# Optimization experiments

Hardware: AMD Instinct MI355X
Metric: run time of the kernel (lower is better)

## Reference

```python
import jax, jax.numpy as jnp
import numpy as np

B, L, S, H = 2, 256, 384, 768
Tc, Dc = 16, 50
WV, WD = 20000, 100
CV = 128
NEG = -1e30


def _lstm_scan(x, Wih, Whh, bih, bhh):
    # x: [N, T, D] -> hs: [N, T, Hc]; torch LSTM gate order i,f,g,o
    N = x.shape[0]
    Hc = Whh.shape[1]
    h0 = jnp.zeros((N, Hc), x.dtype)

    def step(carry, xt):
        h, c = carry
        g = xt @ Wih.T + h @ Whh.T + bih + bhh  # [N, 4Hc]
        i, f, gg, o = jnp.split(g, 4, axis=-1)
        i = jax.nn.sigmoid(i)
        f = jax.nn.sigmoid(f)
        gg = jnp.tanh(gg)
        o = jax.nn.sigmoid(o)
        c = f * c + i * gg
        h = o * jnp.tanh(c)
        return (h, c), h

    _, hs = jax.lax.scan(step, (h0, h0), jnp.swapaxes(x, 0, 1))
    return jnp.swapaxes(hs, 0, 1)


def setup_inputs() -> dict:
    key = jax.random.key(0)
    ks = jax.random.split(key, 10)
    bert_emb = jax.random.normal(ks[0], (B, S, H), jnp.float32)
    pieces2word = jax.random.randint(ks[1], (B, L, S), 0, 2, jnp.int32)
    word_ids = jax.random.randint(ks[2], (B, L), 0, WV, jnp.int32)
    char_count = jax.random.randint(ks[3], (B, L), 1, Tc + 1, jnp.int32)
    char_ids = jax.random.randint(ks[4], (B, L, Tc), 0, CV, jnp.int32)
    # mask consistent with ragged char lengths (first char_count positions valid)
    token_masks_char = (jnp.arange(Tc)[None, None, :] < char_count[..., None]).astype(jnp.int32)
    word_table = jax.random.normal(ks[5], (WV, WD), jnp.float32) * 0.02
    char_table = jax.random.normal(ks[6], (CV, Dc), jnp.float32) * 0.02
    sc = 1.0 / np.sqrt(Dc)

    def lstm_w(k):
        a, b, c, d = jax.random.split(k, 4)
        return (jax.random.uniform(a, (4 * Dc, Dc), jnp.float32, -sc, sc),
                jax.random.uniform(b, (4 * Dc, Dc), jnp.float32, -sc, sc),
                jax.random.uniform(c, (4 * Dc,), jnp.float32, -sc, sc),
                jax.random.uniform(d, (4 * Dc,), jnp.float32, -sc, sc))

    Wih_f, Whh_f, bih_f, bhh_f = lstm_w(ks[7])
    Wih_b, Whh_b, bih_b, bhh_b = lstm_w(ks[8])
    return dict(bert_emb=bert_emb, pieces2word=pieces2word, word_ids=word_ids,
                char_count=char_count, char_ids=char_ids, token_masks_char=token_masks_char,
                word_table=word_table, char_table=char_table,
                Wih_f=Wih_f, Whh_f=Whh_f, bih_f=bih_f, bhh_f=bhh_f,
                Wih_b=Wih_b, Whh_b=Whh_b, bih_b=bih_b, bhh_b=bhh_b)


def reference(bert_emb, pieces2word, word_ids, char_count, char_ids, token_masks_char,
              word_table, char_table, Wih_f, Whh_f, bih_f, bhh_f, Wih_b, Whh_b, bih_b, bhh_b):
    # --- piece2word max pool (expand + masked_fill(min) + max over pieces) ---
    minv = jnp.min(bert_emb)
    # [B, L, S, H] intermediate, as in the original expand
    masked = jnp.where(pieces2word[..., None] != 0, bert_emb[:, None, :, :], minv)
    word_reps = jnp.max(masked, axis=2)  # [B, L, H]
    # dropouts are identity in eval mode

    # --- word embedding lookup ---
    word_embed = word_table[word_ids]  # [B, L, WD]

    # --- char bi-LSTM with packed-sequence semantics ---
    lens = jnp.maximum(char_count.reshape(-1), 1)  # char_count[char_count==0]=1
    x = char_table[char_ids.reshape(B * L, Tc)]  # [N, Tc, Dc]
    h_fwd = _lstm_scan(x, Wih_f, Whh_f, bih_f, bhh_f)
    # reverse each sequence within its valid length for the backward direction
    t = jnp.arange(Tc)[None, :]
    idx = jnp.where(t < lens[:, None], lens[:, None] - 1 - t, t)  # [N, Tc]
    x_rev = jnp.take_along_axis(x, idx[..., None], axis=1)
    h_bwd = _lstm_scan(x_rev, Wih_b, Whh_b, bih_b, bhh_b)
    h_bwd = jnp.take_along_axis(h_bwd, idx[..., None], axis=1)  # back to original order
    h = jnp.concatenate([h_fwd, h_bwd], axis=-1)  # [N, Tc, 2*Dc]
    valid = (t < lens[:, None])[..., None]
    h = jnp.where(valid, h, 0.0)  # pad_packed_sequence zero-pads beyond length
    h = h.reshape(B, L, Tc, 2 * Dc)

    # --- combine(..., 'max'): masked max over ragged char groups ---
    m = jnp.where(token_masks_char[..., None] == 0, NEG, 0.0)
    sup = jnp.max(m + h, axis=2)  # [B, L, 2*Dc]
    sup = jnp.where(sup == NEG, 0.0, sup)

    return jnp.concatenate([word_reps, word_embed, sup], axis=-1)  # [B, L, H+WD+2*Dc]
```

## Files before the change

### kernel.cpp

```cpp
#include <hip/hip_runtime.h>
#include <float.h>

#define Bb 2
#define Ll 256
#define Ss 384
#define Hh 768
#define Tc 16
#define Dc 50
#define WD 100
#define CV 128
#define NG 200
#define OUTC 968


__device__ inline float tanh_fast(float x) {
    float e = __expf(2.f * x);
    return 1.f - 2.f / (e + 1.f);
}
__device__ inline float sigmoid_fast(float x) {
    return 1.f / (1.f + __expf(-x));
}


__global__ __launch_bounds__(256) void kernel1(
        const float* __restrict__ bert, const float* __restrict__ char_table,
        const float* __restrict__ Wih_f, const float* __restrict__ bih_f, const float* __restrict__ bhh_f,
        const float* __restrict__ Wih_b, const float* __restrict__ bih_b, const float* __restrict__ bhh_b,
        float* __restrict__ minp, float* __restrict__ xpt) {
    int blk = blockIdx.x, tid = threadIdx.x;
    if (blk < 128) {
        const int n4 = (Bb * Ss * Hh) / 4;
        const float4* b4 = (const float4*)bert;
        float m = FLT_MAX;
        for (int i = blk * 256 + tid; i < n4; i += 128 * 256) {
            float4 v = b4[i];
            m = fminf(m, fminf(fminf(v.x, v.y), fminf(v.z, v.w)));
        }
        #pragma unroll
        for (int off = 32; off; off >>= 1) m = fminf(m, __shfl_down(m, off, 64));
        __shared__ float red[4];
        if ((tid & 63) == 0) red[tid >> 6] = m;
        __syncthreads();
        if (tid == 0) minp[blk] = fminf(fminf(red[0], red[1]), fminf(red[2], red[3]));
    } else {
        int idx = blk - 128;
        int dir = idx >> 3, c0 = (idx & 7) * 16;
        const float* Wih = dir ? Wih_b : Wih_f;
        const float* bih = dir ? bih_b : bih_f;
        const float* bhh = dir ? bhh_b : bhh_f;
        __shared__ float ct[16][Dc];
        for (int e = tid; e < 16 * Dc; e += 256)
            ((float*)ct)[e] = char_table[c0 * Dc + e];
        __syncthreads();
        if (tid < NG) {
            float w[Dc];
            #pragma unroll
            for (int j = 0; j < Dc; j++) w[j] = Wih[tid * Dc + j];
            float bias = bih[tid] + bhh[tid];
            for (int cid = 0; cid < 16; cid++) {
                float a = bias;
                #pragma unroll
                for (int j = 0; j < Dc; j++) a += w[j] * ct[cid][j];
                xpt[(dir * CV + c0 + cid) * NG + tid] = a;
            }
        }
    }
}


__global__ __launch_bounds__(256, 4) void kernel_lstm(
        const int* __restrict__ char_ids, const int* __restrict__ char_count,
        const float* __restrict__ Whh_f, const float* __restrict__ Whh_b,
        const float* __restrict__ xpt, float* __restrict__ out) {
    __shared__ __align__(16) char smem[13888];
    int blk = blockIdx.x, tid = threadIdx.x;

    float (*xg)[NG] = (float (*)[NG])smem;
    float* gs  = (float*)(smem + 12800);
    float* hs  = (float*)(smem + 13600);
    int*   scid = (int*)(smem + 13808);

    int n = blk >> 1, dir = blk & 1;
    const float* Whh = dir ? Whh_b : Whh_f;

    int len = char_count[n];
    if (len < 1) len = 1;
    if (tid < Tc) {
        int t = tid;
        int st = dir ? (t < len ? len - 1 - t : t) : t;
        scid[t] = char_ids[n * Tc + st];
    }
    if (tid < 52) hs[tid] = 0.f;
    __syncthreads();

    for (int e = tid; e < Tc * (NG / 4); e += 256) {
        int t = e / 50, q = e - t * 50;
        ((float4*)xg[t])[q] = ((const float4*)&xpt[(dir * CV + scid[t]) * NG])[q];
    }
    int wrow = tid < NG ? tid : NG - 1;
    bool istanh = (tid >= 100 && tid < 150);
    float w[52];
    #pragma unroll
    for (int j = 0; j < Dc; j++) w[j] = Whh[wrow * Dc + j];
    w[50] = 0.f; w[51] = 0.f;
    __syncthreads();

    float c = 0.f, maxv = -FLT_MAX;
    for (int t = 0; t < Tc; t++) {
        #pragma unroll
        for (int j = 0; j < 52; j++) asm volatile("" : "+v"(w[j]));
        if (tid < NG) {
            float g = xg[t][tid];
            #pragma unroll
            for (int j = 0; j < 52; j += 4) {
                float4 hv = *(const float4*)&hs[j];
                g += hv.x * w[j] + hv.y * w[j+1] + hv.z * w[j+2] + hv.w * w[j+3];
            }
            gs[tid] = istanh ? tanh_fast(g) : sigmoid_fast(g);
        }
        __syncthreads();
        if (tid < Dc) {
            float si = gs[tid];
            float sf = gs[tid + 50];
            float tg = gs[tid + 100];
            float so = gs[tid + 150];
            c = sf * c + si * tg;
            float h = so * tanh_fast(c);
            hs[tid] = h;
            if (t < len) maxv = fmaxf(maxv, h);
        }
        __syncthreads();
    }
    if (tid < Dc)
        out[(size_t)n * OUTC + (Hh + WD) + dir * Dc + tid] = maxv;
}


__global__ __launch_bounds__(256, 2) void kernel_word(
        const float* __restrict__ bert, const int* __restrict__ p2w,
        const float* __restrict__ minp,
        const int* __restrict__ word_ids, const float* __restrict__ word_table,
        float* __restrict__ out) {
    __shared__ __align__(16) float sm[Ss][8];
    __shared__ __align__(16) float sacc[4][8][128];
    __shared__ float sminv;
    int blk = blockIdx.x, tid = threadIdx.x;

    if (blk < 384) {
        int idx = blk;
        int hc  = idx % 6;
        int lt  = (idx / 6) & 31;
        int b   = idx / 192;
        int l0  = lt * 8;

        const int* pm = p2w + ((size_t)(b * Ll + l0)) * Ss;
        for (int e = tid; e < 8 * Ss; e += 256) {
            int r = e & 7, s = e >> 3;
            sm[s][r] = pm[r * Ss + s] ? 0.f : -FLT_MAX;
        }
        if (tid < 64) {
            float m = fminf(minp[tid], minp[tid + 64]);
            #pragma unroll
            for (int off = 32; off; off >>= 1) m = fminf(m, __shfl_down(m, off, 64));
            if (tid == 0) sminv = m;
        }
        __syncthreads();

        int w    = tid >> 6;
        int lane = tid & 63;
        int s0 = w * 96;

        const float2* bb2 = (const float2*)(bert + (size_t)b * Ss * Hh) + hc * 64 + lane;
        float2 acc[8];
        #pragma unroll
        for (int r = 0; r < 8; r++) { acc[r].x = -FLT_MAX; acc[r].y = -FLT_MAX; }

        for (int jo = 0; jo < 96; jo += 8) {
            float2 v[8];
            #pragma unroll
            for (int k = 0; k < 8; k++) v[k] = bb2[(size_t)(s0 + jo + k) * 384];
            #pragma unroll
            for (int k = 0; k < 8; k++) {
                int j = s0 + jo + k;
                float4 q0 = *(const float4*)&sm[j][0];
                float4 q1 = *(const float4*)&sm[j][4];
                acc[0].x = fmaxf(acc[0].x, v[k].x + q0.x);
                acc[0].y = fmaxf(acc[0].y, v[k].y + q0.x);
                acc[1].x = fmaxf(acc[1].x, v[k].x + q0.y);
                acc[1].y = fmaxf(acc[1].y, v[k].y + q0.y);
                acc[2].x = fmaxf(acc[2].x, v[k].x + q0.z);
                acc[2].y = fmaxf(acc[2].y, v[k].y + q0.z);
                acc[3].x = fmaxf(acc[3].x, v[k].x + q0.w);
                acc[3].y = fmaxf(acc[3].y, v[k].y + q0.w);
                acc[4].x = fmaxf(acc[4].x, v[k].x + q1.x);
                acc[4].y = fmaxf(acc[4].y, v[k].y + q1.x);
                acc[5].x = fmaxf(acc[5].x, v[k].x + q1.y);
                acc[5].y = fmaxf(acc[5].y, v[k].y + q1.y);
                acc[6].x = fmaxf(acc[6].x, v[k].x + q1.z);
                acc[6].y = fmaxf(acc[6].y, v[k].y + q1.z);
                acc[7].x = fmaxf(acc[7].x, v[k].x + q1.w);
                acc[7].y = fmaxf(acc[7].y, v[k].y + q1.w);
            }
        }
        #pragma unroll
        for (int r = 0; r < 8; r++)
            *(float2*)&sacc[w][r][lane * 2] = acc[r];
        __syncthreads();

        float mv = sminv;
        for (int e = tid; e < 8 * 128; e += 256) {
            int r = e >> 7, cx = e & 127;
            float m = fmaxf(fmaxf(sacc[0][r][cx], sacc[1][r][cx]),
                            fmaxf(sacc[2][r][cx], sacc[3][r][cx]));
            if (m == -FLT_MAX) m = mv;
            out[((size_t)(b * Ll + l0 + r)) * OUTC + hc * 128 + cx] = m;
        }
    } else {
        for (int i = (blk - 384) * 256 + tid; i < Bb * Ll * WD; i += 64 * 256) {
            int bl = i / WD, d = i - bl * WD;
            out[(size_t)bl * OUTC + Hh + d] = word_table[(size_t)word_ids[bl] * WD + d];
        }
    }
}

extern "C" void kernel_launch(void* const* d_in, const int* in_sizes, int n_in,
                              void* d_out, int out_size, void* d_ws, size_t ws_size,
                              hipStream_t stream) {
    const float* bert       = (const float*)d_in[0];
    const int*   p2w        = (const int*)d_in[1];
    const int*   word_ids   = (const int*)d_in[2];
    const int*   char_count = (const int*)d_in[3];
    const int*   char_ids   = (const int*)d_in[4];
    const float* word_table = (const float*)d_in[6];
    const float* char_table = (const float*)d_in[7];
    const float* Wih_f = (const float*)d_in[8];
    const float* Whh_f = (const float*)d_in[9];
    const float* bih_f = (const float*)d_in[10];
    const float* bhh_f = (const float*)d_in[11];
    const float* Wih_b = (const float*)d_in[12];
    const float* Whh_b = (const float*)d_in[13];
    const float* bih_b = (const float*)d_in[14];
    const float* bhh_b = (const float*)d_in[15];
    float* out = (float*)d_out;

    float* minp = (float*)d_ws;
    float* xpt  = minp + 128;

    kernel1<<<144, 256, 0, stream>>>(
        bert, char_table, Wih_f, bih_f, bhh_f, Wih_b, bih_b, bhh_b,
        minp, xpt);
    kernel_lstm<<<1024, 256, 0, stream>>>(
        char_ids, char_count, Whh_f, Whh_b, xpt, out);
    kernel_word<<<448, 256, 0, stream>>>(
        bert, p2w, minp, word_ids, word_table, out);
}
```

Measured before the change: 128.7 us.

## Broadcast LSTM hidden state via readlane and halve word-tile rows

Every wavefront in the LSTM recurrence now computes the cell and hidden state redundantly for lanes 0-49. Each thread gets the hidden vector through readlane broadcasts instead of from a shared-memory buffer, which removes one block barrier per time step. The gate buffer is double-buffered so a single barrier per step is enough. The dot product is split across four accumulators. The word max-pool kernel processes 4 words per block instead of 8, doubling the block count for more parallelism, at the cost of reloading bert columns more times.

```diff
diff --git a/kernel.cpp b/kernel.cpp
--- a/kernel.cpp
+++ b/kernel.cpp
@@ -72,25 +72,21 @@
         const int* __restrict__ char_ids, const int* __restrict__ char_count,
         const float* __restrict__ Whh_f, const float* __restrict__ Whh_b,
         const float* __restrict__ xpt, float* __restrict__ out) {
-    __shared__ __align__(16) char smem[13888];
+    __shared__ __align__(16) float xg[Tc][NG];
+    __shared__ __align__(16) float gsb[2][NG];
+    __shared__ int scid[Tc];
+
     int blk = blockIdx.x, tid = threadIdx.x;
-
-    float (*xg)[NG] = (float (*)[NG])smem;
-    float* gs  = (float*)(smem + 12800);
-    float* hs  = (float*)(smem + 13600);
-    int*   scid = (int*)(smem + 13808);
-
     int n = blk >> 1, dir = blk & 1;
     const float* Whh = dir ? Whh_b : Whh_f;
+    int lane = tid & 63;
 
     int len = char_count[n];
     if (len < 1) len = 1;
     if (tid < Tc) {
-        int t = tid;
-        int st = dir ? (t < len ? len - 1 - t : t) : t;
-        scid[t] = char_ids[n * Tc + st];
-    }
-    if (tid < 52) hs[tid] = 0.f;
+        int st = dir ? (tid < len ? len - 1 - tid : tid) : tid;
+        scid[tid] = char_ids[n * Tc + st];
+    }
     __syncthreads();
 
     for (int e = tid; e < Tc * (NG / 4); e += 256) {
@@ -99,63 +95,61 @@
     }
     int wrow = tid < NG ? tid : NG - 1;
     bool istanh = (tid >= 100 && tid < 150);
-    float w[52];
+    float w[50];
     #pragma unroll
-    for (int j = 0; j < Dc; j++) w[j] = Whh[wrow * Dc + j];
-    w[50] = 0.f; w[51] = 0.f;
+    for (int j = 0; j < 50; j++) w[j] = Whh[wrow * 50 + j];
     __syncthreads();
 
-    float c = 0.f, maxv = -FLT_MAX;
+    int ch = lane < 50 ? lane : 49;
+    float c = 0.f, h = 0.f, maxv = -FLT_MAX;
     for (int t = 0; t < Tc; t++) {
-        #pragma unroll
-        for (int j = 0; j < 52; j++) asm volatile("" : "+v"(w[j]));
-        if (tid < NG) {
-            float g = xg[t][tid];
-            #pragma unroll
-            for (int j = 0; j < 52; j += 4) {
-                float4 hv = *(const float4*)&hs[j];
-                g += hv.x * w[j] + hv.y * w[j+1] + hv.z * w[j+2] + hv.w * w[j+3];
-            }
-            gs[tid] = istanh ? tanh_fast(g) : sigmoid_fast(g);
-        }
-        __syncthreads();
-        if (tid < Dc) {
-            float si = gs[tid];
-            float sf = gs[tid + 50];
-            float tg = gs[tid + 100];
-            float so = gs[tid + 150];
-            c = sf * c + si * tg;
-            float h = so * tanh_fast(c);
-            hs[tid] = h;
-            if (t < len) maxv = fmaxf(maxv, h);
-        }
-        __syncthreads();
-    }
-    if (tid < Dc)
+        int hb = __float_as_int(h);
+        float g0 = xg[t][wrow], g1 = 0.f, g2 = 0.f, g3 = 0.f;
+        #pragma unroll
+        for (int j = 0; j < 48; j += 4) {
+            g0 = fmaf(__int_as_float(__builtin_amdgcn_readlane(hb, j)),     w[j],     g0);
+            g1 = fmaf(__int_as_float(__builtin_amdgcn_readlane(hb, j + 1)), w[j + 1], g1);
+            g2 = fmaf(__int_as_float(__builtin_amdgcn_readlane(hb, j + 2)), w[j + 2], g2);
+            g3 = fmaf(__int_as_float(__builtin_amdgcn_readlane(hb, j + 3)), w[j + 3], g3);
+        }
+        g0 = fmaf(__int_as_float(__builtin_amdgcn_readlane(hb, 48)), w[48], g0);
+        g1 = fmaf(__int_as_float(__builtin_amdgcn_readlane(hb, 49)), w[49], g1);
+        float g = (g0 + g1) + (g2 + g3);
+        if (tid < NG)
+            gsb[t & 1][tid] = istanh ? tanh_fast(g) : sigmoid_fast(g);
+        __syncthreads();
+        float si = gsb[t & 1][ch];
+        float sf = gsb[t & 1][ch + 50];
+        float tg = gsb[t & 1][ch + 100];
+        float so = gsb[t & 1][ch + 150];
+        c = sf * c + si * tg;
+        h = so * tanh_fast(c);
+        if (t < len) maxv = fmaxf(maxv, h);
+    }
+    if (tid < 50)
         out[(size_t)n * OUTC + (Hh + WD) + dir * Dc + tid] = maxv;
 }
 
 
-__global__ __launch_bounds__(256, 2) void kernel_word(
+__global__ __launch_bounds__(256) void kernel_word(
         const float* __restrict__ bert, const int* __restrict__ p2w,
         const float* __restrict__ minp,
         const int* __restrict__ word_ids, const float* __restrict__ word_table,
         float* __restrict__ out) {
-    __shared__ __align__(16) float sm[Ss][8];
-    __shared__ __align__(16) float sacc[4][8][128];
+    __shared__ __align__(16) float sm[Ss][4];
+    __shared__ __align__(16) float sacc[4][4][128];
     __shared__ float sminv;
     int blk = blockIdx.x, tid = threadIdx.x;
 
-    if (blk < 384) {
-        int idx = blk;
-        int hc  = idx % 6;
-        int lt  = (idx / 6) & 31;
-        int b   = idx / 192;
-        int l0  = lt * 8;
+    if (blk < 768) {
+        int hc  = blk % 6;
+        int lt  = (blk / 6) & 63;
+        int b   = blk / 384;
+        int l0  = lt * 4;
 
         const int* pm = p2w + ((size_t)(b * Ll + l0)) * Ss;
-        for (int e = tid; e < 8 * Ss; e += 256) {
-            int r = e & 7, s = e >> 3;
+        for (int e = tid; e < 4 * Ss; e += 256) {
+            int r = e / Ss, s = e - r * Ss;
             sm[s][r] = pm[r * Ss + s] ? 0.f : -FLT_MAX;
         }
         if (tid < 64) {
@@ -171,9 +165,9 @@
         int s0 = w * 96;
 
         const float2* bb2 = (const float2*)(bert + (size_t)b * Ss * Hh) + hc * 64 + lane;
-        float2 acc[8];
-        #pragma unroll
-        for (int r = 0; r < 8; r++) { acc[r].x = -FLT_MAX; acc[r].y = -FLT_MAX; }
+        float2 acc[4];
+        #pragma unroll
+        for (int r = 0; r < 4; r++) { acc[r].x = -FLT_MAX; acc[r].y = -FLT_MAX; }
 
         for (int jo = 0; jo < 96; jo += 8) {
             float2 v[8];
@@ -182,33 +176,24 @@
             #pragma unroll
             for (int k = 0; k < 8; k++) {
                 int j = s0 + jo + k;
-                float4 q0 = *(const float4*)&sm[j][0];
-                float4 q1 = *(const float4*)&sm[j][4];
-                acc[0].x = fmaxf(acc[0].x, v[k].x + q0.x);
-                acc[0].y = fmaxf(acc[0].y, v[k].y + q0.x);
-                acc[1].x = fmaxf(acc[1].x, v[k].x + q0.y);
-                acc[1].y = fmaxf(acc[1].y, v[k].y + q0.y);
-                acc[2].x = fmaxf(acc[2].x, v[k].x + q0.z);
-                acc[2].y = fmaxf(acc[2].y, v[k].y + q0.z);
-                acc[3].x = fmaxf(acc[3].x, v[k].x + q0.w);
-                acc[3].y = fmaxf(acc[3].y, v[k].y + q0.w);
-                acc[4].x = fmaxf(acc[4].x, v[k].x + q1.x);
-                acc[4].y = fmaxf(acc[4].y, v[k].y + q1.x);
-                acc[5].x = fmaxf(acc[5].x, v[k].x + q1.y);
-                acc[5].y = fmaxf(acc[5].y, v[k].y + q1.y);
-                acc[6].x = fmaxf(acc[6].x, v[k].x + q1.z);
-                acc[6].y = fmaxf(acc[6].y, v[k].y + q1.z);
-                acc[7].x = fmaxf(acc[7].x, v[k].x + q1.w);
-                acc[7].y = fmaxf(acc[7].y, v[k].y + q1.w);
+                float4 q = *(const float4*)&sm[j][0];
+                acc[0].x = fmaxf(acc[0].x, v[k].x + q.x);
+                acc[0].y = fmaxf(acc[0].y, v[k].y + q.x);
+                acc[1].x = fmaxf(acc[1].x, v[k].x + q.y);
+                acc[1].y = fmaxf(acc[1].y, v[k].y + q.y);
+                acc[2].x = fmaxf(acc[2].x, v[k].x + q.z);
+                acc[2].y = fmaxf(acc[2].y, v[k].y + q.z);
+                acc[3].x = fmaxf(acc[3].x, v[k].x + q.w);
+                acc[3].y = fmaxf(acc[3].y, v[k].y + q.w);
             }
         }
         #pragma unroll
-        for (int r = 0; r < 8; r++)
+        for (int r = 0; r < 4; r++)
             *(float2*)&sacc[w][r][lane * 2] = acc[r];
         __syncthreads();
 
         float mv = sminv;
-        for (int e = tid; e < 8 * 128; e += 256) {
+        for (int e = tid; e < 4 * 128; e += 256) {
             int r = e >> 7, cx = e & 127;
             float m = fmaxf(fmaxf(sacc[0][r][cx], sacc[1][r][cx]),
                             fmaxf(sacc[2][r][cx], sacc[3][r][cx]));
@@ -216,7 +201,7 @@
             out[((size_t)(b * Ll + l0 + r)) * OUTC + hc * 128 + cx] = m;
         }
     } else {
-        for (int i = (blk - 384) * 256 + tid; i < Bb * Ll * WD; i += 64 * 256) {
+        for (int i = (blk - 768) * 256 + tid; i < Bb * Ll * WD; i += 64 * 256) {
             int bl = i / WD, d = i - bl * WD;
             out[(size_t)bl * OUTC + Hh + d] = word_table[(size_t)word_ids[bl] * WD + d];
         }
@@ -251,6 +236,6 @@
         minp, xpt);
     kernel_lstm<<<1024, 256, 0, stream>>>(
         char_ids, char_count, Whh_f, Whh_b, xpt, out);
-    kernel_word<<<448, 256, 0, stream>>>(
+    kernel_word<<<832, 256, 0, stream>>>(
         bert, p2w, minp, word_ids, word_table, out);
 }
```

Result: no change. 129.9 us (+1.0%).
